# Performance work log

Measured on AMD Instinct MI355X. Metric: run time of the kernel, lower is better.

## Reference

```python
import jax, jax.numpy as jnp
import numpy as np

DIM = 1024

def setup_inputs() -> dict:
    key = jax.random.key(0)
    k1, k2, k3, k4, k5 = jax.random.split(key, 5)
    B, S, D = 32, 2048, DIM
    hidden_state = jax.random.normal(k1, (B, D), dtype=jnp.float32)
    encoder_outputs = jax.random.normal(k2, (B, S, D), dtype=jnp.float32)
    # linear1: (2D -> D) with bias; linear2: (D -> 1) no bias
    W1 = jax.random.normal(k3, (2 * D, D), dtype=jnp.float32) / np.sqrt(2 * D)
    b1 = jnp.zeros((D,), dtype=jnp.float32)
    w2 = jax.random.normal(k4, (D,), dtype=jnp.float32) / np.sqrt(D)
    return {"hidden_state": hidden_state, "encoder_outputs": encoder_outputs,
            "W1": W1, "b1": b1, "w2": w2}

def reference(hidden_state, encoder_outputs, W1, b1, w2):
    B, S, D = encoder_outputs.shape
    # concat(encoder_outputs, broadcast hidden) @ W1 == enc @ W1_enc + hid @ W1_hid
    W1_enc, W1_hid = W1[:D], W1[D:]                      # each [D, D]
    enc_proj = jnp.einsum('bsd,de->bse', encoder_outputs, W1_enc)
    hid_proj = jnp.einsum('bd,de->be', hidden_state, W1_hid)
    h = jnp.tanh(enc_proj + hid_proj[:, None, :] + b1)    # [B, S, D]
    e = jnp.einsum('bsd,d->bs', h, w2)                    # [B, S]
    alpha = jax.nn.softmax(e, axis=1)                     # [B, S]
    context = jnp.einsum('bs,bsd->bd', alpha, encoder_outputs)  # [B, D]
    return context
```

## Files before the change

### kernel.cpp

```cpp
#include <hip/hip_runtime.h>
#include <hip/hip_bf16.h>
#include <cstdint>

typedef __bf16 bf16;
typedef __bf16 bf16x8 __attribute__((ext_vector_type(8)));
typedef float  f32x4  __attribute__((ext_vector_type(4)));

#define N_ENCB   0u
#define N_W1BT   134217728u
#define N_C      136314880u
#define N_E      136445952u
#define N_ALPHA  136707072u
#define N_HIDP   136968192u
#define N_CTXP   138016768u
#define N_TOTAL  140113920ull

#define O_W1BT   0u
#define O_C      2097152u
#define O_E      2228224u
#define O_ALPHA  2490368u
#define O_HIDP   2752512u
#define O_CTXP   3801088u

__global__ void k_convert(const float* __restrict__ in, bf16* __restrict__ out) {
    size_t i = ((size_t)blockIdx.x * 256 + threadIdx.x) * 8;
    const size_t stride = (size_t)2048 * 256 * 8;
    for (; i < 67108864ull; i += stride) {
        f32x4 a = *(const f32x4*)(in + i);
        f32x4 b = *(const f32x4*)(in + i + 4);
        bf16x8 o;
        o[0]=(bf16)a[0]; o[1]=(bf16)a[1]; o[2]=(bf16)a[2]; o[3]=(bf16)a[3];
        o[4]=(bf16)b[0]; o[5]=(bf16)b[1]; o[6]=(bf16)b[2]; o[7]=(bf16)b[3];
        *(bf16x8*)(out + i) = o;
    }
}

__global__ void k_cvec_init(const float* __restrict__ b1, float* __restrict__ cvec) {
    int i = blockIdx.x * 256 + threadIdx.x;
    cvec[i] = b1[i & 1023];
}

__global__ void k_hid_atomic(const float* __restrict__ hid, const float* __restrict__ W1,
                             float* __restrict__ cvec) {
    int e = blockIdx.x * 256 + threadIdx.x;
    int dch = blockIdx.y;
    float acc[32];
#pragma unroll
    for (int b = 0; b < 32; ++b) acc[b] = 0.f;
    int d0 = dch * 32;
#pragma unroll 4
    for (int dd = 0; dd < 32; ++dd) {
        int d = d0 + dd;
        float w = W1[(size_t)(1024 + d) * 1024 + e];
#pragma unroll
        for (int b = 0; b < 32; ++b) acc[b] += hid[b * 1024 + d] * w;
    }
#pragma unroll
    for (int b = 0; b < 32; ++b) atomicAdd(&cvec[b * 1024 + e], acc[b]);
}

__global__ void k_hid_partial(const float* __restrict__ hid, const float* __restrict__ W1,
                              float* __restrict__ hidp) {
    int e = blockIdx.x * 256 + threadIdx.x;
    int dch = blockIdx.y;
    float acc[32];
#pragma unroll
    for (int b = 0; b < 32; ++b) acc[b] = 0.f;
    int d0 = dch * 128;
    for (int dd = 0; dd < 128; ++dd) {
        int d = d0 + dd;
        float w = W1[(size_t)(1024 + d) * 1024 + e];
#pragma unroll
        for (int b = 0; b < 32; ++b) acc[b] += hid[b * 1024 + d] * w;
    }
#pragma unroll
    for (int b = 0; b < 32; ++b) hidp[((size_t)dch * 32 + b) * 1024 + e] = acc[b];
}

__global__ void k_hid_reduce(const float* __restrict__ hidp, const float* __restrict__ b1,
                             float* __restrict__ cvec) {
    int i = blockIdx.x * 256 + threadIdx.x;
    int e = i & 1023;
    float s = b1[e];
#pragma unroll
    for (int dch = 0; dch < 8; ++dch) s += hidp[(size_t)dch * 32768 + i];
    cvec[i] = s;
}

__global__ void k_w1t(const float* __restrict__ W1, bf16* __restrict__ w1bt) {
    __shared__ float tile[32][33];
    int tx = threadIdx.x, ty = threadIdx.y;
    int bx = blockIdx.x, by = blockIdx.y;
#pragma unroll
    for (int i = 0; i < 4; ++i)
        tile[ty + i * 8][tx] = W1[(size_t)(by * 32 + ty + i * 8) * 1024 + bx * 32 + tx];
    __syncthreads();
#pragma unroll
    for (int i = 0; i < 4; ++i)
        w1bt[(size_t)(bx * 32 + ty + i * 8) * 1024 + by * 32 + tx] = (bf16)tile[tx][ty + i * 8];
}

__device__ inline float fast_tanh(float x) {
    float e2 = __expf(2.f * x);
    return 1.f - 2.f / (e2 + 1.f);
}

#define SBAR  __builtin_amdgcn_s_barrier()
#define LGKM0 asm volatile("s_waitcnt lgkmcnt(0)" ::: "memory")
#define VMC4  asm volatile("s_waitcnt vmcnt(4)" ::: "memory")
#define PRIO1 __builtin_amdgcn_s_setprio(1)
#define PRIO0 __builtin_amdgcn_s_setprio(0)

template<int D, int MH>
__device__ __forceinline__ void rdA(const char* pA0, const char* pA1, bf16x8 (&bA)[4][2]) {
#pragma unroll
    for (int m = 0; m < 4; ++m) {
        bA[m][0] = *(const bf16x8*)(pA0 + D * 32768 + MH * 8192 + m * 2048);
        bA[m][1] = *(const bf16x8*)(pA1 + D * 32768 + MH * 8192 + m * 2048);
    }
}
template<int D, int N0>
__device__ __forceinline__ void rdB(const char* pB0, const char* pB1, bf16x8 (&bB)[4][2]) {
#pragma unroll
    for (int n = 0; n < 2; ++n) {
        bB[N0 + n][0] = *(const bf16x8*)(pB0 + D * 32768 + (N0 + n) * 2048);
        bB[N0 + n][1] = *(const bf16x8*)(pB1 + D * 32768 + (N0 + n) * 2048);
    }
}
template<int MH, int NH>
__device__ __forceinline__ void mfmaQ(bf16x8 (&bA)[4][2], bf16x8 (&bB)[4][2], f32x4 (&acc)[8][4]) {
#pragma unroll
    for (int kk = 0; kk < 2; ++kk)
#pragma unroll
        for (int m = 0; m < 4; ++m)
#pragma unroll
            for (int n = 0; n < 2; ++n)
                acc[MH * 4 + m][NH * 2 + n] = __builtin_amdgcn_mfma_f32_16x16x32_bf16(
                    bA[m][kk], bB[NH * 2 + n][kk], acc[MH * 4 + m][NH * 2 + n], 0, 0, 0);
}

__global__ __launch_bounds__(512, 1) void k_gemm8(
    const bf16* __restrict__ encb, const bf16* __restrict__ w1bt,
    const float* __restrict__ cvec, const float* __restrict__ w2,
    float* __restrict__ ebuf)
{
    __shared__ __align__(16) char smem[131072];
    const int t = threadIdx.x;
    const int lane = t & 63;
    const int w  = t >> 6;
    const int wr = w >> 2;
    const int wc = w & 3;
    const int l15 = lane & 15, g = (lane >> 4) & 3;

    unsigned bidx = blockIdx.x;
    unsigned swz0 = (bidx & 7u) * 128u + (bidx >> 3);
    const int nt  = swz0 & 3;
    const int mt0 = swz0 >> 2;
    const int n0  = nt * 256;

    const int r6  = t >> 3;
    const int gsl = (t & 7) ^ (r6 & 7);
    const char* srcA    = (const char*)encb + (size_t)(mt0 * 256 + r6) * 2048 + gsl * 16;
    const char* srcA_nx = srcA + (size_t)2048 * 2048;
    const char* srcB    = (const char*)w1bt + (size_t)(n0 + r6) * 2048 + gsl * 16;

#define STAGE_A(SRC, D, H, KT) do { \
    const char* _s = (SRC) + (size_t)(H) * 262144 + (size_t)(KT) * 128; \
    __builtin_amdgcn_global_load_lds((const __attribute__((address_space(1))) unsigned int*)_s, \
        (__attribute__((address_space(3))) unsigned int*)(smem + (D) * 32768 + (H) * 16384 + w * 1024), 16, 0, 0); \
    __builtin_amdgcn_global_load_lds((const __attribute__((address_space(1))) unsigned int*)(_s + 131072), \
        (__attribute__((address_space(3))) unsigned int*)(smem + (D) * 32768 + (H) * 16384 + 8192 + w * 1024), 16, 0, 0); \
} while (0)
#define STAGE_B(D, H, KT) do { \
    const char* _s = srcB + (size_t)(H) * 262144 + (size_t)(KT) * 128; \
    __builtin_amdgcn_global_load_lds((const __attribute__((address_space(1))) unsigned int*)_s, \
        (__attribute__((address_space(3))) unsigned int*)(smem + 65536 + (D) * 32768 + (H) * 16384 + w * 1024), 16, 0, 0); \
    __builtin_amdgcn_global_load_lds((const __attribute__((address_space(1))) unsigned int*)(_s + 131072), \
        (__attribute__((address_space(3))) unsigned int*)(smem + 65536 + (D) * 32768 + (H) * 16384 + 8192 + w * 1024), 16, 0, 0); \
} while (0)

    const int rbA = wr * 128 + l15;
    const int rbB = wc * 64 + l15;
    const int sK0 = (g ^ (l15 & 7)) << 4;
    const int sK1 = sK0 ^ 64;
    const char* pA0 = smem + rbA * 128 + sK0;
    const char* pA1 = smem + rbA * 128 + sK1;
    const char* pB0 = smem + 65536 + rbB * 128 + sK0;
    const char* pB1 = smem + 65536 + rbB * 128 + sK1;

    f32x4 acc[8][4] = {};
    bf16x8 bA[4][2], bB[4][2];

    float wv[4];
    int gcol[4];
#pragma unroll
    for (int n = 0; n < 4; ++n) {
        gcol[n] = n0 + wc * 64 + n * 16 + l15;
        wv[n] = w2[gcol[n]];
    }

    STAGE_A(srcA, 0, 0, 0); STAGE_A(srcA, 0, 1, 0);
    STAGE_B(0, 0, 0); STAGE_B(0, 1, 0);
    STAGE_B(1, 0, 1); STAGE_B(1, 1, 1);
    VMC4; SBAR;

#pragma unroll 1
    for (int j = 0; j < 4; ++j) {
#pragma unroll 1
        for (int i = 0; i < 8; ++i) {
            const int st1 = 2 * i + 1;
            const bool last = (i == 7);
            const int st2 = last ? 0 : 2 * i + 2;
            const int st3 = last ? 1 : 2 * i + 3;
            const char* sA2 = last ? ((j < 3) ? srcA_nx : srcA) : srcA;

            rdA<0, 0>(pA0, pA1, bA); rdB<0, 0>(pB0, pB1, bB);
            STAGE_A(srcA, 1, 0, st1);
            SBAR; LGKM0; PRIO1; mfmaQ<0, 0>(bA, bB, acc); PRIO0; SBAR;
            rdB<0, 2>(pB0, pB1, bB);
            STAGE_A(srcA, 1, 1, st1);
            SBAR; LGKM0; PRIO1; mfmaQ<0, 1>(bA, bB, acc); PRIO0; SBAR;
            rdA<0, 1>(pA0, pA1, bA);
            STAGE_B(0, 0, st2);
            SBAR; LGKM0; PRIO1; mfmaQ<1, 0>(bA, bB, acc); PRIO0; SBAR;
            STAGE_B(0, 1, st2);
            SBAR; LGKM0; PRIO1; mfmaQ<1, 1>(bA, bB, acc); PRIO0; VMC4; SBAR;
            rdA<1, 0>(pA0, pA1, bA); rdB<1, 0>(pB0, pB1, bB);
            STAGE_A(sA2, 0, 0, st2);
            SBAR; LGKM0; PRIO1; mfmaQ<0, 0>(bA, bB, acc); PRIO0; SBAR;
            rdB<1, 2>(pB0, pB1, bB);
            STAGE_A(sA2, 0, 1, st2);
            SBAR; LGKM0; PRIO1; mfmaQ<0, 1>(bA, bB, acc); PRIO0; SBAR;
            rdA<1, 1>(pA0, pA1, bA);
            STAGE_B(1, 0, st3);
            SBAR; LGKM0; PRIO1; mfmaQ<1, 0>(bA, bB, acc); PRIO0; SBAR;
            STAGE_B(1, 1, st3);
            SBAR; LGKM0; PRIO1; mfmaQ<1, 1>(bA, bB, acc); PRIO0; VMC4; SBAR;
        }

        const int m0j = (mt0 + 8 * j) * 256;
        const int bj  = m0j >> 11;
        float cv[4];
#pragma unroll
        for (int n = 0; n < 4; ++n) cv[n] = cvec[bj * 1024 + gcol[n]];
#pragma unroll
        for (int m = 0; m < 8; ++m) {
#pragma unroll
            for (int r = 0; r < 4; ++r) {
                float s = 0.f;
#pragma unroll
                for (int n = 0; n < 4; ++n)
                    s += fast_tanh(acc[m][n][r] + cv[n]) * wv[n];
                s += __shfl_xor(s, 1); s += __shfl_xor(s, 2);
                s += __shfl_xor(s, 4); s += __shfl_xor(s, 8);
                if (l15 == 0)
                    atomicAdd(&ebuf[m0j + wr * 128 + m * 16 + g * 4 + r], s);
            }
        }
#pragma unroll
        for (int m = 0; m < 8; ++m)
#pragma unroll
            for (int n = 0; n < 4; ++n)
                acc[m][n] = f32x4{0.f, 0.f, 0.f, 0.f};

        srcA = srcA_nx;
        srcA_nx += (size_t)2048 * 2048;
    }
#undef STAGE_A
#undef STAGE_B
}

__global__ __launch_bounds__(256, 3) void k_gemm_e(
    const float* __restrict__ enc, const bf16* __restrict__ w1bt,
    const float* __restrict__ cvec, const float* __restrict__ w2,
    float* __restrict__ ebuf)
{
    __shared__ __align__(16) unsigned char smem[24 * 1024];
    const int t = threadIdx.x;
    const int lane = t & 63;
    const int w = t >> 6;
    const int wr = w >> 1, wc = w & 1;
    const int l15 = lane & 15, g = lane >> 4;

    unsigned raw = blockIdx.x;
    unsigned swz = (raw & 7u) * 512u + (raw >> 3);
    const int nt = swz & 7, mt = swz >> 3;
    const int m0 = mt * 128, n0 = nt * 128;
    const int b = m0 >> 11;

    int rowA = (t >> 3);
    int slotA = (t & 7) ^ (rowA & 7);
    const char* gA0 = (const char*)enc + (size_t)(m0 + rowA) * 4096 + slotA * 16;
    int rowB = (t >> 2);
    int slotB = (t & 3) ^ ((t >> 3) & 3);
    const char* gB0 = (const char*)w1bt + (size_t)(n0 + rowB) * 2048 + slotB * 16;

    int rowA0 = wr * 64 + l15;
    unsigned offA0 = (unsigned)rowA0 * 128 + ((((2 * g)) ^ (l15 & 7)) << 4);
    int rowB0 = wc * 64 + l15;
    unsigned offB0 = 16384u + (unsigned)rowB0 * 64 + (((g ^ ((l15 >> 1) & 3))) << 4);

    f32x4 acc[4][4] = {};

    for (int kt = 0; kt < 32; ++kt) {
        const char* pa = gA0 + kt * 128;
        const char* pb = gB0 + kt * 64;
#pragma unroll
        for (int c = 0; c < 4; ++c)
            __builtin_amdgcn_global_load_lds(
                (const __attribute__((address_space(1))) unsigned int*)(pa + (size_t)c * 131072),
                (__attribute__((address_space(3))) unsigned int*)(smem + c * 4096 + w * 1024), 16, 0, 0);
#pragma unroll
        for (int c = 0; c < 2; ++c)
            __builtin_amdgcn_global_load_lds(
                (const __attribute__((address_space(1))) unsigned int*)(pb + (size_t)c * 131072),
                (__attribute__((address_space(3))) unsigned int*)(smem + 16384 + c * 4096 + w * 1024), 16, 0, 0);
        __syncthreads();

        bf16x8 af[4], bfr[4];
#pragma unroll
        for (int m = 0; m < 4; ++m) {
            unsigned o0 = offA0 + m * 2048;
            f32x4 lo = *(const f32x4*)(smem + o0);
            f32x4 hi = *(const f32x4*)(smem + (o0 ^ 16u));
            bf16x8 a;
            a[0] = (bf16)lo[0]; a[1] = (bf16)lo[1]; a[2] = (bf16)lo[2]; a[3] = (bf16)lo[3];
            a[4] = (bf16)hi[0]; a[5] = (bf16)hi[1]; a[6] = (bf16)hi[2]; a[7] = (bf16)hi[3];
            af[m] = a;
        }
#pragma unroll
        for (int n = 0; n < 4; ++n)
            bfr[n] = *(const bf16x8*)(smem + (offB0 + n * 1024));
#pragma unroll
        for (int m = 0; m < 4; ++m)
#pragma unroll
            for (int n = 0; n < 4; ++n)
                acc[m][n] = __builtin_amdgcn_mfma_f32_16x16x32_bf16(af[m], bfr[n], acc[m][n], 0, 0, 0);
        __syncthreads();
    }

    float cv[4], wv[4];
#pragma unroll
    for (int n = 0; n < 4; ++n) {
        int gcol = n0 + wc * 64 + n * 16 + l15;
        cv[n] = cvec[b * 1024 + gcol];
        wv[n] = w2[gcol];
    }
#pragma unroll
    for (int m = 0; m < 4; ++m) {
#pragma unroll
        for (int r = 0; r < 4; ++r) {
            float s = 0.f;
#pragma unroll
            for (int n = 0; n < 4; ++n)
                s += fast_tanh(acc[m][n][r] + cv[n]) * wv[n];
            s += __shfl_xor(s, 1); s += __shfl_xor(s, 2);
            s += __shfl_xor(s, 4); s += __shfl_xor(s, 8);
            if (l15 == 0)
                atomicAdd(&ebuf[m0 + wr * 64 + m * 16 + g * 4 + r], s);
        }
    }
}

__global__ void k_softmax(const float* __restrict__ ebuf, float* __restrict__ alpha) {
    int bb = blockIdx.x, t = threadIdx.x;
    __shared__ float red[4], red2[4];
    float v[8];
    float mx = -1e30f;
#pragma unroll
    for (int i = 0; i < 8; ++i) { v[i] = ebuf[bb * 2048 + i * 256 + t]; mx = fmaxf(mx, v[i]); }
    for (int o = 32; o > 0; o >>= 1) mx = fmaxf(mx, __shfl_xor(mx, o));
    if ((t & 63) == 0) red[t >> 6] = mx;
    __syncthreads();
    mx = fmaxf(fmaxf(red[0], red[1]), fmaxf(red[2], red[3]));
    float sum = 0.f;
#pragma unroll
    for (int i = 0; i < 8; ++i) { v[i] = __expf(v[i] - mx); sum += v[i]; }
    for (int o = 32; o > 0; o >>= 1) sum += __shfl_xor(sum, o);
    if ((t & 63) == 0) red2[t >> 6] = sum;
    __syncthreads();
    sum = red2[0] + red2[1] + red2[2] + red2[3];
    float inv = 1.f / sum;
#pragma unroll
    for (int i = 0; i < 8; ++i) alpha[bb * 2048 + i * 256 + t] = v[i] * inv;
}

__global__ void k_ctx_partial(const float* __restrict__ enc, const float* __restrict__ alpha,
                              float* __restrict__ ctxp) {
    int bid = blockIdx.x;
    int bb = bid >> 4, sc = bid & 15;
    int t = threadIdx.x;
    __shared__ float al[128];
    if (t < 128) al[t] = alpha[bb * 2048 + sc * 128 + t];
    __syncthreads();
    f32x4 acc = {0.f, 0.f, 0.f, 0.f};
    const f32x4* base = (const f32x4*)(enc + ((size_t)bb * 2048 + sc * 128) * 1024) + t;
    for (int s = 0; s < 128; ++s) {
        f32x4 vv = base[(size_t)s * 256];
        acc += vv * al[s];
    }
    *((f32x4*)(ctxp + (size_t)bid * 1024) + t) = acc;
}

__global__ void k_ctx_reduce(const float* __restrict__ ctxp, float* __restrict__ out) {
    int i = blockIdx.x * 256 + threadIdx.x;
    int bb = i >> 10, d = i & 1023;
    float s = 0.f;
#pragma unroll
    for (int sc = 0; sc < 16; ++sc) s += ctxp[((size_t)(bb * 16 + sc)) * 1024 + d];
    out[i] = s;
}

extern "C" void kernel_launch(void* const* d_in, const int* in_sizes, int n_in,
                              void* d_out, int out_size, void* d_ws, size_t ws_size,
                              hipStream_t stream) {
    const float* hid = (const float*)d_in[0];
    const float* enc = (const float*)d_in[1];
    const float* W1  = (const float*)d_in[2];
    const float* b1  = (const float*)d_in[3];
    const float* w2  = (const float*)d_in[4];
    float* out = (float*)d_out;
    char* ws = (char*)d_ws;

    if (ws_size >= N_TOTAL) {
        bf16*  encb  = (bf16*)(ws + N_ENCB);
        bf16*  w1bt  = (bf16*)(ws + N_W1BT);
        float* cvec  = (float*)(ws + N_C);
        float* ebuf  = (float*)(ws + N_E);
        float* alpha = (float*)(ws + N_ALPHA);
        float* ctxp  = (float*)(ws + N_CTXP);

        hipMemsetAsync(ebuf, 0, 65536 * sizeof(float), stream);
        k_convert<<<2048, 256, 0, stream>>>(enc, encb);
        k_w1t<<<dim3(32, 32), dim3(32, 8), 0, stream>>>(W1, w1bt);
        k_cvec_init<<<128, 256, 0, stream>>>(b1, cvec);
        k_hid_atomic<<<dim3(4, 32), 256, 0, stream>>>(hid, W1, cvec);
        k_gemm8<<<256, 512, 0, stream>>>(encb, w1bt, cvec, w2, ebuf);
        k_softmax<<<32, 256, 0, stream>>>(ebuf, alpha);
        k_ctx_partial<<<512, 256, 0, stream>>>(enc, alpha, ctxp);
        k_ctx_reduce<<<128, 256, 0, stream>>>(ctxp, out);
    } else {
        bf16*  w1bt  = (bf16*)(ws + O_W1BT);
        float* cvec  = (float*)(ws + O_C);
        float* ebuf  = (float*)(ws + O_E);
        float* alpha = (float*)(ws + O_ALPHA);
        float* hidp  = (float*)(ws + O_HIDP);
        float* ctxp  = (float*)(ws + O_CTXP);

        hipMemsetAsync(ebuf, 0, 65536 * sizeof(float), stream);
        k_hid_partial<<<dim3(4, 8), 256, 0, stream>>>(hid, W1, hidp);
        k_w1t<<<dim3(32, 32), dim3(32, 8), 0, stream>>>(W1, w1bt);
        k_hid_reduce<<<128, 256, 0, stream>>>(hidp, b1, cvec);
        k_gemm_e<<<4096, 256, 0, stream>>>(enc, w1bt, cvec, w2, ebuf);
        k_softmax<<<32, 256, 0, stream>>>(ebuf, alpha);
        k_ctx_partial<<<512, 256, 0, stream>>>(enc, alpha, ctxp);
        k_ctx_reduce<<<128, 256, 0, stream>>>(ctxp, out);
    }
}
```

Measured before the change: 292.1 us.

## Read bf16 encoder copy for context and coarsen GEMM barrier schedule

The context partial-sum kernel now reads the bf16 encoder copy already produced for the GEMM instead of the fp32 input. This halves the bytes streamed in that bandwidth-bound pass, at the cost of bf16 rounding in the context output. In the main GEMM loop, the explicit lgkmcnt(0) waits are removed and pairs of MFMA quads are merged between barriers, so there are half as many s_barriers per iteration. The risk is fewer sync points for LDS staging hazards and a different overlap of LDS reads with MFMA work.

```diff
diff --git a/kernel.cpp b/kernel.cpp
--- a/kernel.cpp
+++ b/kernel.cpp
@@ -106,7 +106,6 @@
 }
 
 #define SBAR  __builtin_amdgcn_s_barrier()
-#define LGKM0 asm volatile("s_waitcnt lgkmcnt(0)" ::: "memory")
 #define VMC4  asm volatile("s_waitcnt vmcnt(4)" ::: "memory")
 #define PRIO1 __builtin_amdgcn_s_setprio(1)
 #define PRIO0 __builtin_amdgcn_s_setprio(0)
@@ -214,28 +213,35 @@
             const int st3 = last ? 1 : 2 * i + 3;
             const char* sA2 = last ? ((j < 3) ? srcA_nx : srcA) : srcA;
 
-            rdA<0, 0>(pA0, pA1, bA); rdB<0, 0>(pB0, pB1, bB);
+            rdA<0, 0>(pA0, pA1, bA);
+            rdB<0, 0>(pB0, pB1, bB);
+            rdB<0, 2>(pB0, pB1, bB);
             STAGE_A(srcA, 1, 0, st1);
-            SBAR; LGKM0; PRIO1; mfmaQ<0, 0>(bA, bB, acc); PRIO0; SBAR;
-            rdB<0, 2>(pB0, pB1, bB);
             STAGE_A(srcA, 1, 1, st1);
-            SBAR; LGKM0; PRIO1; mfmaQ<0, 1>(bA, bB, acc); PRIO0; SBAR;
+            PRIO1; mfmaQ<0, 0>(bA, bB, acc); mfmaQ<0, 1>(bA, bB, acc); PRIO0;
+            SBAR;
+
             rdA<0, 1>(pA0, pA1, bA);
             STAGE_B(0, 0, st2);
-            SBAR; LGKM0; PRIO1; mfmaQ<1, 0>(bA, bB, acc); PRIO0; SBAR;
             STAGE_B(0, 1, st2);
-            SBAR; LGKM0; PRIO1; mfmaQ<1, 1>(bA, bB, acc); PRIO0; VMC4; SBAR;
-            rdA<1, 0>(pA0, pA1, bA); rdB<1, 0>(pB0, pB1, bB);
+            PRIO1; mfmaQ<1, 0>(bA, bB, acc); mfmaQ<1, 1>(bA, bB, acc); PRIO0;
+            VMC4;
+            SBAR;
+
+            rdA<1, 0>(pA0, pA1, bA);
+            rdB<1, 0>(pB0, pB1, bB);
+            rdB<1, 2>(pB0, pB1, bB);
             STAGE_A(sA2, 0, 0, st2);
-            SBAR; LGKM0; PRIO1; mfmaQ<0, 0>(bA, bB, acc); PRIO0; SBAR;
-            rdB<1, 2>(pB0, pB1, bB);
             STAGE_A(sA2, 0, 1, st2);
-            SBAR; LGKM0; PRIO1; mfmaQ<0, 1>(bA, bB, acc); PRIO0; SBAR;
+            PRIO1; mfmaQ<0, 0>(bA, bB, acc); mfmaQ<0, 1>(bA, bB, acc); PRIO0;
+            SBAR;
+
             rdA<1, 1>(pA0, pA1, bA);
             STAGE_B(1, 0, st3);
-            SBAR; LGKM0; PRIO1; mfmaQ<1, 0>(bA, bB, acc); PRIO0; SBAR;
             STAGE_B(1, 1, st3);
-            SBAR; LGKM0; PRIO1; mfmaQ<1, 1>(bA, bB, acc); PRIO0; VMC4; SBAR;
+            PRIO1; mfmaQ<1, 0>(bA, bB, acc); mfmaQ<1, 1>(bA, bB, acc); PRIO0;
+            VMC4;
+            SBAR;
         }
 
         const int m0j = (mt0 + 8 * j) * 256;
@@ -385,6 +391,37 @@
     for (int i = 0; i < 8; ++i) alpha[bb * 2048 + i * 256 + t] = v[i] * inv;
 }
 
+__global__ void k_ctx_partial_b(const bf16* __restrict__ encb, const float* __restrict__ alpha,
+                                float* __restrict__ ctxp) {
+    int bid = blockIdx.x;
+    int bb = bid >> 4, sc = bid & 15;
+    int t = threadIdx.x;
+    __shared__ float al[128];
+    __shared__ float red[128 * 8];
+    if (t < 128) al[t] = alpha[bb * 2048 + sc * 128 + t];
+    __syncthreads();
+    int d0 = (t & 127) * 8;
+    int sp = t >> 7;
+    float acc[8] = {};
+    const bf16* base = encb + ((size_t)bb * 2048 + sc * 128 + sp) * 1024 + d0;
+    for (int s = 0; s < 128; s += 2) {
+        bf16x8 v = *(const bf16x8*)(base + (size_t)s * 1024);
+        float a = al[s + sp];
+#pragma unroll
+        for (int k = 0; k < 8; ++k) acc[k] += a * (float)v[k];
+    }
+    if (sp == 1) {
+#pragma unroll
+        for (int k = 0; k < 8; ++k) red[(t & 127) * 8 + k] = acc[k];
+    }
+    __syncthreads();
+    if (sp == 0) {
+        float* o = ctxp + (size_t)bid * 1024 + d0;
+#pragma unroll
+        for (int k = 0; k < 8; ++k) o[k] = acc[k] + red[t * 8 + k];
+    }
+}
+
 __global__ void k_ctx_partial(const float* __restrict__ enc, const float* __restrict__ alpha,
                               float* __restrict__ ctxp) {
     int bid = blockIdx.x;
@@ -437,7 +474,7 @@
         k_hid_atomic<<<dim3(4, 32), 256, 0, stream>>>(hid, W1, cvec);
         k_gemm8<<<256, 512, 0, stream>>>(encb, w1bt, cvec, w2, ebuf);
         k_softmax<<<32, 256, 0, stream>>>(ebuf, alpha);
-        k_ctx_partial<<<512, 256, 0, stream>>>(enc, alpha, ctxp);
+        k_ctx_partial_b<<<512, 256, 0, stream>>>(encb, alpha, ctxp);
         k_ctx_reduce<<<128, 256, 0, stream>>>(ctxp, out);
     } else {
         bf16*  w1bt  = (bf16*)(ws + O_W1BT);
```

New measurement: 263.6 us, median of 2. 9.8% less time.
